# Optimization experiments

Measured on AMD Instinct MI355X. Metric: run time of the kernel, lower is better.

## Reference

```python
import jax, jax.numpy as jnp
import numpy as np
import math

B, N, CS, CZ = 1, 1024, 384, 128
H, G, PQ, PV = 8, 16, 8, 12
C = 3 * G              # c_hidden = group_dim * 3 = 48
CZ4 = CZ // 4
INF, EPS = 1e5, 1e-8


def _quat_to_rot(q):
    # q: [..., 4] -> [..., 3, 3] valid rotation matrices
    q = q / jnp.linalg.norm(q, axis=-1, keepdims=True)
    w, x, y, z = q[..., 0], q[..., 1], q[..., 2], q[..., 3]
    r = jnp.stack([
        1 - 2 * (y * y + z * z), 2 * (x * y - w * z), 2 * (x * z + w * y),
        2 * (x * y + w * z), 1 - 2 * (x * x + z * z), 2 * (y * z - w * x),
        2 * (x * z - w * y), 2 * (y * z + w * x), 1 - 2 * (x * x + y * y)], axis=-1)
    return r.reshape(q.shape[:-1] + (3, 3))


def setup_inputs() -> dict:
    key = jax.random.key(0)
    ks = jax.random.split(key, 12)
    sc = lambda d: 1.0 / math.sqrt(d)
    inp = {
        's': jax.random.normal(ks[0], (B, N, CS), jnp.float32),
        'z': jax.random.normal(ks[1], (B, N, N, CZ), jnp.float32),
        'rot': _quat_to_rot(jax.random.normal(ks[2], (B, N, 4), jnp.float32)),
        'mask': jnp.ones((B, N), jnp.float32),
        'wq': jax.random.normal(ks[3], (CS, H * C), jnp.float32) * sc(CS),
        'bq': jnp.zeros((H * C,), jnp.float32),
        'wkv': jax.random.normal(ks[4], (CS, 2 * H * C), jnp.float32) * sc(CS),
        'bkv': jnp.zeros((2 * H * C,), jnp.float32),
        'wkvp': jax.random.normal(ks[5], (CS, H * (PQ + PV) * 3), jnp.float32) * sc(CS),
        'bkvp': jnp.zeros((H * (PQ + PV) * 3,), jnp.float32),
        'wb': jax.random.normal(ks[6], (CZ, H), jnp.float32) * sc(CZ),
        'bb': jnp.zeros((H,), jnp.float32),
        'wdz': jax.random.normal(ks[7], (CZ, CZ4), jnp.float32) * sc(CZ),
        'bdz': jnp.zeros((CZ4,), jnp.float32),
        'wout': jax.random.normal(ks[8], (H * (CZ4 + C + 4 * PV), CS), jnp.float32) * sc(H * (CZ4 + C + 4 * PV)),
        'bout': jnp.zeros((CS,), jnp.float32),
        # ipa_point_weights_init_ -> softplus_inverse(1.0) = log(e-1); add jitter
        'gw': jnp.full((G,), float(np.log(np.e - 1.0)), jnp.float32) + 0.1 * jax.random.normal(ks[9], (G,), jnp.float32),
    }
    return inp


def reference(s, z, rot, mask, wq, bq, wkv, bkv, wkvp, bkvp, wb, bb, wdz, bdz, wout, bout, gw):
    # scalar q/k/v: [B,N,H,C]
    q = (s @ wq + bq).reshape(B, N, H, C)
    kv = (s @ wkv + bkv).reshape(B, N, H, 2 * C)
    k, v = kv[..., :C], kv[..., C:]

    # kv points: split last dim into 3 coordinate chunks, stack on -1 (per source)
    kvp = (s @ wkvp + bkvp).reshape(B, N, 3, H * (PQ + PV))
    kvp = jnp.moveaxis(kvp, -2, -1).reshape(B, N, H, PQ + PV, 3)
    v_pts = kvp[..., PQ:, :]  # [B,N,H,PV,3]; note: NOT rigid-transformed in source

    # pair bias [B,N,N,H]
    b = z @ wb + bb

    # groupwise 3D-RoPE: rotate per-residue 3D groups by frame rotation
    q_rot = jnp.einsum('bnij,bnhgj->bnhgi', rot, q.reshape(B, N, H, G, 3))
    k_rot = jnp.einsum('bnij,bnhgj->bnhgi', rot, k.reshape(B, N, H, G, 3))
    gs = jnp.einsum('bnhgi,bmhgi->bhgnm', q_rot, k_rot) / math.sqrt(3.0)  # [B,H,G,N,N]
    hw = jax.nn.softplus(gw) * math.sqrt(1.0 / G)  # [G]
    a = jnp.einsum('bhgnm,g->bhnm', gs, hw)
    a = a + math.sqrt(1.0 / 3.0) * jnp.transpose(b, (0, 3, 1, 2))

    sq_mask = INF * (mask[:, :, None] * mask[:, None, :] - 1.0)  # [B,N,N]
    a = jax.nn.softmax(a + sq_mask[:, None], axis=-1)  # [B,H,N,N]

    # scalar output
    o = jnp.einsum('bhnm,bmhc->bnhc', a, v).reshape(B, N, H * C)
    # point output
    o_pt = jnp.einsum('bhnm,bmhpc->bnhpc', a, v_pts)  # [B,N,H,PV,3]
    o_pt_norm = jnp.sqrt(jnp.sum(o_pt ** 2, axis=-1) + EPS).reshape(B, N, H * PV)
    o_pt = o_pt.reshape(B, N, H * PV, 3)
    # pair output
    pair_z = z @ wdz + bdz  # [B,N,N,CZ4]
    o_pair = jnp.einsum('bhnm,bnmd->bnhd', a, pair_z).reshape(B, N, H * CZ4)

    feats = jnp.concatenate([o, o_pt[..., 0], o_pt[..., 1], o_pt[..., 2], o_pt_norm, o_pair], axis=-1)
    return feats @ wout + bout
```

## Files before the change

### kernel.cpp

```cpp
#include <hip/hip_runtime.h>
#include <math.h>

#define NRES 1024
#define HH 8
#define CC 48
#define CZF 128

__global__ __launch_bounds__(256) void k_proj(
    const float* __restrict__ s,
    const float* __restrict__ wq, const float* __restrict__ bq,
    const float* __restrict__ wkv, const float* __restrict__ bkv,
    const float* __restrict__ wkvp, const float* __restrict__ bkvp,
    float* __restrict__ raw)
{
  int bb = blockIdx.x;
  int n0 = (bb >> 1) * 8;
  int ch = bb & 1;
  int t = threadIdx.x;
  const float* srow = s + (size_t)n0 * 384;
  for (int ci = 0; ci < 4; ci++) {
    int local = ci * 256 + t;
    if (local >= 816) break;
    int col = ch * 816 + local;
    const float* w; int ld; float bias;
    if (col < 384)       { w = wq  + col;          ld = 384; bias = bq[col]; }
    else if (col < 1152) { w = wkv + (col - 384);  ld = 768; bias = bkv[col - 384]; }
    else                 { w = wkvp + (col - 1152); ld = 480; bias = bkvp[col - 1152]; }
    float acc[8];
#pragma unroll
    for (int r = 0; r < 8; r++) acc[r] = bias;
    for (int k = 0; k < 384; k++) {
      float wv = w[(size_t)k * ld];
#pragma unroll
      for (int r = 0; r < 8; r++) acc[r] = fmaf(srow[r * 384 + k], wv, acc[r]);
    }
#pragma unroll
    for (int r = 0; r < 8; r++) raw[(size_t)(n0 + r) * 1632 + col] = acc[r];
  }
}

__global__ __launch_bounds__(256) void k_scatter(
    const float* __restrict__ raw, const float* __restrict__ rot,
    const float* __restrict__ gw,
    float* __restrict__ qp, float* __restrict__ kp, float* __restrict__ V2)
{
  int n = blockIdx.x, t = threadIdx.x;
  __shared__ float rsh[1632];
  __shared__ float hwsh[16];
  for (int i = t; i < 1632; i += 256) rsh[i] = raw[(size_t)n * 1632 + i];
  if (t < 16) hwsh[t] = log1pf(expf(gw[t])) * 0.25f;
  __syncthreads();
  float r00 = rot[n*9+0], r01 = rot[n*9+1], r02 = rot[n*9+2];
  float r10 = rot[n*9+3], r11 = rot[n*9+4], r12 = rot[n*9+5];
  float r20 = rot[n*9+6], r21 = rot[n*9+7], r22 = rot[n*9+8];
  for (int idx = t; idx < 768; idx += 256) {
    int isK = idx >= 384;
    int rem = idx - (isK ? 384 : 0);
    int h = rem / 48, gi = rem % 48, g = gi / 3, ii = gi % 3;
    int cb = isK ? (384 + h * 96 + g * 3) : (h * 48 + g * 3);
    float x = rsh[cb], y = rsh[cb + 1], zz = rsh[cb + 2];
    float d0 = r00 * x + r01 * y + r02 * zz;
    float d1 = r10 * x + r11 * y + r12 * zz;
    float d2 = r20 * x + r21 * y + r22 * zz;
    float val = (ii == 0) ? d0 : (ii == 1 ? d1 : d2);
    if (!isK) {
      val *= hwsh[g] * 0.57735026919f;
      qp[(size_t)((h << 10) + n) * 48 + gi] = val;
    } else {
      kp[(size_t)((h << 10) + n) * 48 + gi] = val;
    }
  }
  for (int idx = t; idx < 768; idx += 256) {
    int h = idx / 96, c = idx % 96;
    float val = 0.f;
    if (c < 48) val = rsh[384 + h * 96 + 48 + c];
    else if (c < 84) {
      int pc = c - 48, pp = pc / 3, j = pc % 3;
      val = rsh[1152 + j * 160 + h * 20 + 8 + pp];
    }
    V2[(size_t)((h << 10) + n) * 96 + c] = val;
  }
}

__global__ __launch_bounds__(256) void k_bias(
    const float* __restrict__ z, const float* __restrict__ wb,
    const float* __restrict__ bb, const float* __restrict__ mask,
    float* __restrict__ S)
{
  __shared__ float zsh[8192];
  __shared__ float wbrep[4128];
  __shared__ float bbsh[8];
  int t = threadIdx.x;
  size_t pair0 = (size_t)blockIdx.x * 64;
  for (int idx = t; idx < 1024; idx += 256) {
    float v = wb[idx];
    wbrep[idx] = v; wbrep[1032 + idx] = v; wbrep[2064 + idx] = v; wbrep[3096 + idx] = v;
  }
  if (t < 8) bbsh[t] = bb[t];
  const float4* z4 = (const float4*)(z + pair0 * 128);
#pragma unroll
  for (int it = 0; it < 8; it++) {
    int idx = it * 256 + t;
    float4 f = z4[idx];
    int r = idx >> 5, c = (idx & 31) * 4;
    *(float4*)&zsh[r * 128 + ((c + 4 * r) & 127)] = f;
  }
  __syncthreads();
  int q = t & 3, r = t >> 2;
  float acc[8];
#pragma unroll
  for (int hh = 0; hh < 8; hh++) acc[hh] = 0.f;
  const float* wbq = wbrep + q * 1032;
#pragma unroll
  for (int i = 0; i < 8; i++) {
    int c = q * 4 + i * 16;
    float4 zf = *(const float4*)&zsh[r * 128 + ((c + 4 * r) & 127)];
#pragma unroll
    for (int j = 0; j < 4; j++) {
      float zv = (j == 0) ? zf.x : (j == 1) ? zf.y : (j == 2) ? zf.z : zf.w;
      float4 w0 = *(const float4*)&wbq[(c + j) * 8];
      float4 w1 = *(const float4*)&wbq[(c + j) * 8 + 4];
      acc[0] = fmaf(zv, w0.x, acc[0]); acc[1] = fmaf(zv, w0.y, acc[1]);
      acc[2] = fmaf(zv, w0.z, acc[2]); acc[3] = fmaf(zv, w0.w, acc[3]);
      acc[4] = fmaf(zv, w1.x, acc[4]); acc[5] = fmaf(zv, w1.y, acc[5]);
      acc[6] = fmaf(zv, w1.z, acc[6]); acc[7] = fmaf(zv, w1.w, acc[7]);
    }
  }
#pragma unroll
  for (int hh = 0; hh < 8; hh++) {
    acc[hh] += __shfl_xor(acc[hh], 1, 64);
    acc[hh] += __shfl_xor(acc[hh], 2, 64);
  }
  size_t pair = pair0 + r;
  int n = (int)(pair >> 10), m = (int)(pair & 1023);
  float mt = 100000.0f * (mask[n] * mask[m] - 1.0f);
  const float is3 = 0.57735026919f;
  int h0 = q * 2;
  S[(size_t)h0 * 1048576 + pair]       = (acc[h0] + bbsh[h0]) * is3 + mt;
  S[(size_t)(h0 + 1) * 1048576 + pair] = (acc[h0 + 1] + bbsh[h0 + 1]) * is3 + mt;
}

__global__ __launch_bounds__(256) void k_attn(
    const float* __restrict__ qp, const float* __restrict__ kp,
    float* __restrict__ S)
{
  int b = blockIdx.x;
  int h = b >> 7, n0 = (b & 127) * 8;
  int t = threadIdx.x;
  __shared__ float ksh[128 * 52];
  __shared__ float ssh[8 * 1024];
  int ms = t & 127, nh = t >> 7;
  const float* qbase = qp + (size_t)((h << 10) + n0 + nh * 4) * 48;
  size_t Sbase = (size_t)h * 1048576 + (size_t)n0 * 1024;
  for (int cb = 0; cb < 1024; cb += 128) {
    __syncthreads();
    for (int idx = t; idx < 1536; idx += 256) {
      int r = idx / 12, p = idx % 12;
      float4 f = *(const float4*)(kp + (size_t)((h << 10) + cb + r) * 48 + p * 4);
      *(float4*)&ksh[r * 52 + p * 4] = f;
    }
    __syncthreads();
    int m = cb + ms;
    float a0 = 0.f, a1 = 0.f, a2 = 0.f, a3 = 0.f;
#pragma unroll
    for (int ic = 0; ic < 12; ic++) {
      float4 kf = *(const float4*)&ksh[ms * 52 + ic * 4];
      float4 q0 = *(const float4*)(qbase + 0 * 48 + ic * 4);
      float4 q1 = *(const float4*)(qbase + 1 * 48 + ic * 4);
      float4 q2 = *(const float4*)(qbase + 2 * 48 + ic * 4);
      float4 q3 = *(const float4*)(qbase + 3 * 48 + ic * 4);
      a0 += q0.x * kf.x + q0.y * kf.y + q0.z * kf.z + q0.w * kf.w;
      a1 += q1.x * kf.x + q1.y * kf.y + q1.z * kf.z + q1.w * kf.w;
      a2 += q2.x * kf.x + q2.y * kf.y + q2.z * kf.z + q2.w * kf.w;
      a3 += q3.x * kf.x + q3.y * kf.y + q3.z * kf.z + q3.w * kf.w;
    }
    int rb = nh * 4;
    ssh[(rb + 0) * 1024 + m] = a0 + S[Sbase + (size_t)(rb + 0) * 1024 + m];
    ssh[(rb + 1) * 1024 + m] = a1 + S[Sbase + (size_t)(rb + 1) * 1024 + m];
    ssh[(rb + 2) * 1024 + m] = a2 + S[Sbase + (size_t)(rb + 2) * 1024 + m];
    ssh[(rb + 3) * 1024 + m] = a3 + S[Sbase + (size_t)(rb + 3) * 1024 + m];
  }
  __syncthreads();
  int row = t >> 5, lane = t & 31;
  float* sr = ssh + row * 1024;
  float mx = -1e30f;
  for (int j = lane; j < 1024; j += 32) mx = fmaxf(mx, sr[j]);
#pragma unroll
  for (int o = 16; o >= 1; o >>= 1) mx = fmaxf(mx, __shfl_xor(mx, o, 32));
  float sum = 0.f;
  for (int j = lane; j < 1024; j += 32) {
    float e = __expf(sr[j] - mx);
    sr[j] = e; sum += e;
  }
#pragma unroll
  for (int o = 16; o >= 1; o >>= 1) sum += __shfl_xor(sum, o, 32);
  float inv = 1.0f / sum;
  float* Sout = S + Sbase + (size_t)row * 1024;
  for (int j = lane; j < 1024; j += 32) Sout[j] = sr[j] * inv;
}

__global__ __launch_bounds__(256) void k_av(
    const float* __restrict__ S, const float* __restrict__ V2,
    float* __restrict__ F)
{
  int b = blockIdx.x;
  int h = b >> 6, n0 = (b & 63) * 16;
  int t = threadIdx.x;
  __shared__ float as2[64 * 20];
  __shared__ float fsh[16 * 96];
  int np = t >> 5, c4 = t & 31;
  float4 a0 = {0,0,0,0}, a1 = {0,0,0,0};
  size_t Sbase = (size_t)h * 1048576 + (size_t)n0 * 1024;
  for (int mc = 0; mc < 1024; mc += 64) {
    __syncthreads();
    for (int idx = t; idx < 1024; idx += 256) {
      int mm = idx & 63, nn = idx >> 6;
      as2[mm * 20 + nn] = S[Sbase + (size_t)nn * 1024 + mc + mm];
    }
    __syncthreads();
    if (c4 < 24) {
      const float* vbase = V2 + (size_t)((h << 10) + mc) * 96 + c4 * 4;
      for (int mm = 0; mm < 64; mm++) {
        float4 vv = *(const float4*)(vbase + mm * 96);
        float2 av = *(const float2*)&as2[mm * 20 + np * 2];
        a0.x += av.x * vv.x; a0.y += av.x * vv.y; a0.z += av.x * vv.z; a0.w += av.x * vv.w;
        a1.x += av.y * vv.x; a1.y += av.y * vv.y; a1.z += av.y * vv.z; a1.w += av.y * vv.w;
      }
    }
  }
  if (c4 < 24) {
    *(float4*)&fsh[(np * 2 + 0) * 96 + c4 * 4] = a0;
    *(float4*)&fsh[(np * 2 + 1) * 96 + c4 * 4] = a1;
  }
  __syncthreads();
  for (int idx = t; idx < 768; idx += 256) {
    int nn = idx / 48, c = idx % 48;
    F[(size_t)(n0 + nn) * 1024 + h * 48 + c] = fsh[nn * 96 + c];
  }
  for (int idx = t; idx < 192; idx += 256) {
    int nn = idx / 12, pp = idx % 12;
    float x = fsh[nn * 96 + 48 + pp * 3];
    float y = fsh[nn * 96 + 48 + pp * 3 + 1];
    float zz = fsh[nn * 96 + 48 + pp * 3 + 2];
    size_t base = (size_t)(n0 + nn) * 1024;
    F[base + 384 + h * 12 + pp] = x;
    F[base + 480 + h * 12 + pp] = y;
    F[base + 576 + h * 12 + pp] = zz;
    F[base + 672 + h * 12 + pp] = sqrtf(x * x + y * y + zz * zz + 1e-8f);
  }
}

__global__ __launch_bounds__(256) void k_az(
    const float* __restrict__ S, const float* __restrict__ z,
    float* __restrict__ tmp)
{
  int n = blockIdx.x, t = threadIdx.x;
  __shared__ float zsh[8192];
  __shared__ float as2[64 * 12];
  int mg = t >> 5, c4 = t & 31;
  float4 acc[8];
#pragma unroll
  for (int hh = 0; hh < 8; hh++) acc[hh] = {0,0,0,0};
  for (int mc = 0; mc < 1024; mc += 64) {
    __syncthreads();
    const float4* z4 = (const float4*)(z + ((size_t)n * 1024 + mc) * 128);
#pragma unroll
    for (int it = 0; it < 8; it++) {
      int idx = it * 256 + t;
      float4 f = z4[idx];
      int r = idx >> 5, c = (idx & 31) * 4;
      *(float4*)&zsh[r * 128 + ((c + 4 * r) & 127)] = f;
    }
    for (int idx = t; idx < 512; idx += 256) {
      int mm = idx & 63, hh = idx >> 6;
      as2[mm * 12 + hh] = S[(size_t)hh * 1048576 + (size_t)n * 1024 + mc + mm];
    }
    __syncthreads();
#pragma unroll
    for (int k2 = 0; k2 < 8; k2++) {
      int mm = mg + k2 * 8;
      float4 zf = *(const float4*)&zsh[mm * 128 + ((c4 * 4 + 4 * mm) & 127)];
      float4 av0 = *(const float4*)&as2[mm * 12];
      float4 av1 = *(const float4*)&as2[mm * 12 + 4];
      acc[0].x += av0.x*zf.x; acc[0].y += av0.x*zf.y; acc[0].z += av0.x*zf.z; acc[0].w += av0.x*zf.w;
      acc[1].x += av0.y*zf.x; acc[1].y += av0.y*zf.y; acc[1].z += av0.y*zf.z; acc[1].w += av0.y*zf.w;
      acc[2].x += av0.z*zf.x; acc[2].y += av0.z*zf.y; acc[2].z += av0.z*zf.z; acc[2].w += av0.z*zf.w;
      acc[3].x += av0.w*zf.x; acc[3].y += av0.w*zf.y; acc[3].z += av0.w*zf.z; acc[3].w += av0.w*zf.w;
      acc[4].x += av1.x*zf.x; acc[4].y += av1.x*zf.y; acc[4].z += av1.x*zf.z; acc[4].w += av1.x*zf.w;
      acc[5].x += av1.y*zf.x; acc[5].y += av1.y*zf.y; acc[5].z += av1.y*zf.z; acc[5].w += av1.y*zf.w;
      acc[6].x += av1.z*zf.x; acc[6].y += av1.z*zf.y; acc[6].z += av1.z*zf.z; acc[6].w += av1.z*zf.w;
      acc[7].x += av1.w*zf.x; acc[7].y += av1.w*zf.y; acc[7].z += av1.w*zf.z; acc[7].w += av1.w*zf.w;
    }
  }
  __syncthreads();
#pragma unroll
  for (int hh = 0; hh < 8; hh++)
    *(float4*)&zsh[mg * 1024 + hh * 128 + c4 * 4] = acc[hh];
  __syncthreads();
  for (int idx = t; idx < 1024; idx += 256) {
    float sv = 0.f;
#pragma unroll
    for (int g2 = 0; g2 < 8; g2++) sv += zsh[g2 * 1024 + idx];
    tmp[(size_t)n * 1024 + idx] = sv;
  }
}

__global__ __launch_bounds__(256) void k_out(
    const float* __restrict__ F, const float* __restrict__ tmp,
    const float* __restrict__ wdz, const float* __restrict__ bdz,
    const float* __restrict__ wout, const float* __restrict__ bout,
    float* __restrict__ out)
{
  int n0 = blockIdx.x * 4, t = threadIdx.x;
  __shared__ float fsh[4 * 1024];
  for (int idx = t; idx < 3072; idx += 256) {
    int nn = idx / 768, c = idx % 768;
    fsh[nn * 1024 + c] = F[(size_t)(n0 + nn) * 1024 + c];
  }
  {
    int h = t >> 5, d = t & 31;
#pragma unroll
    for (int nn = 0; nn < 4; nn++) {
      float acc = bdz[d];
      const float* tr = tmp + (size_t)(n0 + nn) * 1024 + h * 128;
      for (int c = 0; c < 128; c++) acc = fmaf(tr[c], wdz[c * 32 + d], acc);
      fsh[nn * 1024 + 768 + h * 32 + d] = acc;
    }
  }
  __syncthreads();
  int j = t & 127, kh = t >> 7;
  float a[3][4];
#pragma unroll
  for (int jj = 0; jj < 3; jj++)
#pragma unroll
    for (int r = 0; r < 4; r++) a[jj][r] = 0.f;
  const float4* f4p = (const float4*)fsh;
  for (int k4 = kh * 128; k4 < kh * 128 + 128; k4++) {
    float4 f0 = f4p[0 * 256 + k4];
    float4 f1 = f4p[1 * 256 + k4];
    float4 f2 = f4p[2 * 256 + k4];
    float4 f3 = f4p[3 * 256 + k4];
    int k = k4 * 4;
#pragma unroll
    for (int u = 0; u < 4; u++) {
      float w0 = wout[(size_t)(k + u) * 384 + j];
      float w1 = wout[(size_t)(k + u) * 384 + j + 128];
      float w2 = wout[(size_t)(k + u) * 384 + j + 256];
      float e0 = (u == 0) ? f0.x : (u == 1) ? f0.y : (u == 2) ? f0.z : f0.w;
      float e1 = (u == 0) ? f1.x : (u == 1) ? f1.y : (u == 2) ? f1.z : f1.w;
      float e2 = (u == 0) ? f2.x : (u == 1) ? f2.y : (u == 2) ? f2.z : f2.w;
      float e3 = (u == 0) ? f3.x : (u == 1) ? f3.y : (u == 2) ? f3.z : f3.w;
      a[0][0] = fmaf(e0, w0, a[0][0]); a[0][1] = fmaf(e1, w0, a[0][1]);
      a[0][2] = fmaf(e2, w0, a[0][2]); a[0][3] = fmaf(e3, w0, a[0][3]);
      a[1][0] = fmaf(e0, w1, a[1][0]); a[1][1] = fmaf(e1, w1, a[1][1]);
      a[1][2] = fmaf(e2, w1, a[1][2]); a[1][3] = fmaf(e3, w1, a[1][3]);
      a[2][0] = fmaf(e0, w2, a[2][0]); a[2][1] = fmaf(e1, w2, a[2][1]);
      a[2][2] = fmaf(e2, w2, a[2][2]); a[2][3] = fmaf(e3, w2, a[2][3]);
    }
  }
  __syncthreads();
  if (kh == 1) {
#pragma unroll
    for (int jj = 0; jj < 3; jj++)
#pragma unroll
      for (int r = 0; r < 4; r++)
        fsh[(jj * 4 + r) * 128 + j] = a[jj][r];
  }
  __syncthreads();
  if (kh == 0) {
#pragma unroll
    for (int jj = 0; jj < 3; jj++)
#pragma unroll
      for (int r = 0; r < 4; r++) {
        float v = a[jj][r] + fsh[(jj * 4 + r) * 128 + j] + bout[jj * 128 + j];
        out[(size_t)(n0 + r) * 384 + jj * 128 + j] = v;
      }
  }
}

extern "C" void kernel_launch(void* const* d_in, const int* in_sizes, int n_in,
                              void* d_out, int out_size, void* d_ws, size_t ws_size,
                              hipStream_t stream) {
  const float* s    = (const float*)d_in[0];
  const float* z    = (const float*)d_in[1];
  const float* rot  = (const float*)d_in[2];
  const float* mask = (const float*)d_in[3];
  const float* wq   = (const float*)d_in[4];
  const float* bq   = (const float*)d_in[5];
  const float* wkv  = (const float*)d_in[6];
  const float* bkv  = (const float*)d_in[7];
  const float* wkvp = (const float*)d_in[8];
  const float* bkvp = (const float*)d_in[9];
  const float* wb   = (const float*)d_in[10];
  const float* bb   = (const float*)d_in[11];
  const float* wdz  = (const float*)d_in[12];
  const float* bdz  = (const float*)d_in[13];
  const float* wout = (const float*)d_in[14];
  const float* bout = (const float*)d_in[15];
  const float* gw   = (const float*)d_in[16];
  float* out = (float*)d_out;

  float* ws  = (float*)d_ws;
  float* raw = ws;
  float* qp  = raw + 1024 * 1632;
  float* kp  = qp + 393216;
  float* V2  = kp + 393216;
  float* S   = V2 + 786432;
  float* tmp = S + 8388608;
  float* F   = tmp + 1048576;

  k_proj<<<256, 256, 0, stream>>>(s, wq, bq, wkv, bkv, wkvp, bkvp, raw);
  k_scatter<<<1024, 256, 0, stream>>>(raw, rot, gw, qp, kp, V2);
  k_bias<<<16384, 256, 0, stream>>>(z, wb, bb, mask, S);
  k_attn<<<1024, 256, 0, stream>>>(qp, kp, S);
  k_av<<<512, 256, 0, stream>>>(S, V2, F);
  k_az<<<1024, 256, 0, stream>>>(S, z, tmp);
  k_out<<<256, 256, 0, stream>>>(F, tmp, wdz, bdz, wout, bout, out);
}
```

Baseline: 1.326 ms.

## Rework grids and staging across proj, bias, av, az and out kernels

Splits k_proj and k_out over twice as many blocks to raise parallelism. k_bias now reads z straight from global memory instead of staging it through shared memory, with each thread handling four pairs, and shrinks the replicated weight table. k_av stages the whole attention row block transposed in LDS once, and k_az stages all head attention weights once and streams z directly from global, which removes the per-chunk barriers. The bigger LDS footprint in k_av (about 74KB) lowers occupancy, and the direct global z loads give up the coalesced shared-memory staging.

```diff
diff --git a/kernel.cpp b/kernel.cpp
--- a/kernel.cpp
+++ b/kernel.cpp
@@ -14,14 +14,14 @@
     float* __restrict__ raw)
 {
   int bb = blockIdx.x;
-  int n0 = (bb >> 1) * 8;
-  int ch = bb & 1;
+  int n0 = (bb >> 2) * 8;
+  int ch = bb & 3;
   int t = threadIdx.x;
   const float* srow = s + (size_t)n0 * 384;
-  for (int ci = 0; ci < 4; ci++) {
+  for (int ci = 0; ci < 2; ci++) {
     int local = ci * 256 + t;
-    if (local >= 816) break;
-    int col = ch * 816 + local;
+    if (local >= 408) break;
+    int col = ch * 408 + local;
     const float* w; int ld; float bias;
     if (col < 384)       { w = wq  + col;          ld = 384; bias = bq[col]; }
     else if (col < 1152) { w = wkv + (col - 384);  ld = 768; bias = bkv[col - 384]; }
@@ -87,57 +87,74 @@
     const float* __restrict__ bb, const float* __restrict__ mask,
     float* __restrict__ S)
 {
-  __shared__ float zsh[8192];
-  __shared__ float wbrep[4128];
+  __shared__ float wbrep[2][1032];
   __shared__ float bbsh[8];
   int t = threadIdx.x;
-  size_t pair0 = (size_t)blockIdx.x * 64;
+  size_t pair0 = (size_t)blockIdx.x * 256;
   for (int idx = t; idx < 1024; idx += 256) {
     float v = wb[idx];
-    wbrep[idx] = v; wbrep[1032 + idx] = v; wbrep[2064 + idx] = v; wbrep[3096 + idx] = v;
+    wbrep[0][idx] = v; wbrep[1][idx] = v;
   }
   if (t < 8) bbsh[t] = bb[t];
-  const float4* z4 = (const float4*)(z + pair0 * 128);
-#pragma unroll
-  for (int it = 0; it < 8; it++) {
-    int idx = it * 256 + t;
-    float4 f = z4[idx];
-    int r = idx >> 5, c = (idx & 31) * 4;
-    *(float4*)&zsh[r * 128 + ((c + 4 * r) & 127)] = f;
-  }
   __syncthreads();
   int q = t & 3, r = t >> 2;
-  float acc[8];
-#pragma unroll
-  for (int hh = 0; hh < 8; hh++) acc[hh] = 0.f;
-  const float* wbq = wbrep + q * 1032;
+  const float* wbq = wbrep[q >> 1];
+  float acc[4][8];
+#pragma unroll
+  for (int g = 0; g < 4; g++)
+#pragma unroll
+    for (int hh = 0; hh < 8; hh++) acc[g][hh] = 0.f;
+  const float* zb = z + (pair0 + r) * 128;
 #pragma unroll
   for (int i = 0; i < 8; i++) {
     int c = q * 4 + i * 16;
-    float4 zf = *(const float4*)&zsh[r * 128 + ((c + 4 * r) & 127)];
+    float4 zf0 = *(const float4*)(zb + (size_t)0 * 8192 + c);
+    float4 zf1 = *(const float4*)(zb + (size_t)1 * 8192 + c);
+    float4 zf2 = *(const float4*)(zb + (size_t)2 * 8192 + c);
+    float4 zf3 = *(const float4*)(zb + (size_t)3 * 8192 + c);
 #pragma unroll
     for (int j = 0; j < 4; j++) {
-      float zv = (j == 0) ? zf.x : (j == 1) ? zf.y : (j == 2) ? zf.z : zf.w;
       float4 w0 = *(const float4*)&wbq[(c + j) * 8];
       float4 w1 = *(const float4*)&wbq[(c + j) * 8 + 4];
-      acc[0] = fmaf(zv, w0.x, acc[0]); acc[1] = fmaf(zv, w0.y, acc[1]);
-      acc[2] = fmaf(zv, w0.z, acc[2]); acc[3] = fmaf(zv, w0.w, acc[3]);
-      acc[4] = fmaf(zv, w1.x, acc[4]); acc[5] = fmaf(zv, w1.y, acc[5]);
-      acc[6] = fmaf(zv, w1.z, acc[6]); acc[7] = fmaf(zv, w1.w, acc[7]);
-    }
-  }
-#pragma unroll
-  for (int hh = 0; hh < 8; hh++) {
-    acc[hh] += __shfl_xor(acc[hh], 1, 64);
-    acc[hh] += __shfl_xor(acc[hh], 2, 64);
-  }
-  size_t pair = pair0 + r;
-  int n = (int)(pair >> 10), m = (int)(pair & 1023);
-  float mt = 100000.0f * (mask[n] * mask[m] - 1.0f);
+      float z0 = (j == 0) ? zf0.x : (j == 1) ? zf0.y : (j == 2) ? zf0.z : zf0.w;
+      float z1 = (j == 0) ? zf1.x : (j == 1) ? zf1.y : (j == 2) ? zf1.z : zf1.w;
+      float z2 = (j == 0) ? zf2.x : (j == 1) ? zf2.y : (j == 2) ? zf2.z : zf2.w;
+      float z3 = (j == 0) ? zf3.x : (j == 1) ? zf3.y : (j == 2) ? zf3.z : zf3.w;
+      acc[0][0] = fmaf(z0, w0.x, acc[0][0]); acc[0][1] = fmaf(z0, w0.y, acc[0][1]);
+      acc[0][2] = fmaf(z0, w0.z, acc[0][2]); acc[0][3] = fmaf(z0, w0.w, acc[0][3]);
+      acc[0][4] = fmaf(z0, w1.x, acc[0][4]); acc[0][5] = fmaf(z0, w1.y, acc[0][5]);
+      acc[0][6] = fmaf(z0, w1.z, acc[0][6]); acc[0][7] = fmaf(z0, w1.w, acc[0][7]);
+      acc[1][0] = fmaf(z1, w0.x, acc[1][0]); acc[1][1] = fmaf(z1, w0.y, acc[1][1]);
+      acc[1][2] = fmaf(z1, w0.z, acc[1][2]); acc[1][3] = fmaf(z1, w0.w, acc[1][3]);
+      acc[1][4] = fmaf(z1, w1.x, acc[1][4]); acc[1][5] = fmaf(z1, w1.y, acc[1][5]);
+      acc[1][6] = fmaf(z1, w1.z, acc[1][6]); acc[1][7] = fmaf(z1, w1.w, acc[1][7]);
+      acc[2][0] = fmaf(z2, w0.x, acc[2][0]); acc[2][1] = fmaf(z2, w0.y, acc[2][1]);
+      acc[2][2] = fmaf(z2, w0.z, acc[2][2]); acc[2][3] = fmaf(z2, w0.w, acc[2][3]);
+      acc[2][4] = fmaf(z2, w1.x, acc[2][4]); acc[2][5] = fmaf(z2, w1.y, acc[2][5]);
+      acc[2][6] = fmaf(z2, w1.z, acc[2][6]); acc[2][7] = fmaf(z2, w1.w, acc[2][7]);
+      acc[3][0] = fmaf(z3, w0.x, acc[3][0]); acc[3][1] = fmaf(z3, w0.y, acc[3][1]);
+      acc[3][2] = fmaf(z3, w0.z, acc[3][2]); acc[3][3] = fmaf(z3, w0.w, acc[3][3]);
+      acc[3][4] = fmaf(z3, w1.x, acc[3][4]); acc[3][5] = fmaf(z3, w1.y, acc[3][5]);
+      acc[3][6] = fmaf(z3, w1.z, acc[3][6]); acc[3][7] = fmaf(z3, w1.w, acc[3][7]);
+    }
+  }
+#pragma unroll
+  for (int g = 0; g < 4; g++)
+#pragma unroll
+    for (int hh = 0; hh < 8; hh++) {
+      acc[g][hh] += __shfl_xor(acc[g][hh], 1, 64);
+      acc[g][hh] += __shfl_xor(acc[g][hh], 2, 64);
+    }
   const float is3 = 0.57735026919f;
   int h0 = q * 2;
-  S[(size_t)h0 * 1048576 + pair]       = (acc[h0] + bbsh[h0]) * is3 + mt;
-  S[(size_t)(h0 + 1) * 1048576 + pair] = (acc[h0 + 1] + bbsh[h0 + 1]) * is3 + mt;
+#pragma unroll
+  for (int g = 0; g < 4; g++) {
+    size_t pair = pair0 + r + (size_t)g * 64;
+    int n = (int)(pair >> 10), m = (int)(pair & 1023);
+    float mt = 100000.0f * (mask[n] * mask[m] - 1.0f);
+    S[(size_t)h0 * 1048576 + pair]       = (acc[g][h0] + bbsh[h0]) * is3 + mt;
+    S[(size_t)(h0 + 1) * 1048576 + pair] = (acc[g][h0 + 1] + bbsh[h0 + 1]) * is3 + mt;
+  }
 }
 
 __global__ __launch_bounds__(256) void k_attn(
@@ -206,29 +223,25 @@
   int b = blockIdx.x;
   int h = b >> 6, n0 = (b & 63) * 16;
   int t = threadIdx.x;
-  __shared__ float as2[64 * 20];
+  __shared__ float asT[1024 * 18];
   __shared__ float fsh[16 * 96];
+  size_t Sbase = (size_t)h * 1048576 + (size_t)n0 * 1024;
+  for (int idx = t; idx < 16384; idx += 256) {
+    int nn = idx >> 10, m = idx & 1023;
+    asT[m * 18 + nn] = S[Sbase + (size_t)nn * 1024 + m];
+  }
+  __syncthreads();
   int np = t >> 5, c4 = t & 31;
   float4 a0 = {0,0,0,0}, a1 = {0,0,0,0};
-  size_t Sbase = (size_t)h * 1048576 + (size_t)n0 * 1024;
-  for (int mc = 0; mc < 1024; mc += 64) {
-    __syncthreads();
-    for (int idx = t; idx < 1024; idx += 256) {
-      int mm = idx & 63, nn = idx >> 6;
-      as2[mm * 20 + nn] = S[Sbase + (size_t)nn * 1024 + mc + mm];
-    }
-    __syncthreads();
-    if (c4 < 24) {
-      const float* vbase = V2 + (size_t)((h << 10) + mc) * 96 + c4 * 4;
-      for (int mm = 0; mm < 64; mm++) {
-        float4 vv = *(const float4*)(vbase + mm * 96);
-        float2 av = *(const float2*)&as2[mm * 20 + np * 2];
-        a0.x += av.x * vv.x; a0.y += av.x * vv.y; a0.z += av.x * vv.z; a0.w += av.x * vv.w;
-        a1.x += av.y * vv.x; a1.y += av.y * vv.y; a1.z += av.y * vv.z; a1.w += av.y * vv.w;
-      }
-    }
-  }
   if (c4 < 24) {
+    const float* vbase = V2 + (size_t)(h << 10) * 96 + c4 * 4;
+#pragma unroll 4
+    for (int mm = 0; mm < 1024; mm++) {
+      float4 vv = *(const float4*)(vbase + (size_t)mm * 96);
+      float2 av = *(const float2*)&asT[mm * 18 + np * 2];
+      a0.x += av.x * vv.x; a0.y += av.x * vv.y; a0.z += av.x * vv.z; a0.w += av.x * vv.w;
+      a1.x += av.y * vv.x; a1.y += av.y * vv.y; a1.z += av.y * vv.z; a1.w += av.y * vv.w;
+    }
     *(float4*)&fsh[(np * 2 + 0) * 96 + c4 * 4] = a0;
     *(float4*)&fsh[(np * 2 + 1) * 96 + c4 * 4] = a1;
   }
@@ -255,52 +268,41 @@
     float* __restrict__ tmp)
 {
   int n = blockIdx.x, t = threadIdx.x;
-  __shared__ float zsh[8192];
-  __shared__ float as2[64 * 12];
+  __shared__ float ash[8192];
   int mg = t >> 5, c4 = t & 31;
+  for (int idx = t; idx < 8192; idx += 256) {
+    int hh = idx >> 10, m = idx & 1023;
+    ash[m * 8 + hh] = S[(size_t)hh * 1048576 + (size_t)n * 1024 + m];
+  }
+  __syncthreads();
   float4 acc[8];
 #pragma unroll
-  for (int hh = 0; hh < 8; hh++) acc[hh] = {0,0,0,0};
-  for (int mc = 0; mc < 1024; mc += 64) {
-    __syncthreads();
-    const float4* z4 = (const float4*)(z + ((size_t)n * 1024 + mc) * 128);
-#pragma unroll
-    for (int it = 0; it < 8; it++) {
-      int idx = it * 256 + t;
-      float4 f = z4[idx];
-      int r = idx >> 5, c = (idx & 31) * 4;
-      *(float4*)&zsh[r * 128 + ((c + 4 * r) & 127)] = f;
-    }
-    for (int idx = t; idx < 512; idx += 256) {
-      int mm = idx & 63, hh = idx >> 6;
-      as2[mm * 12 + hh] = S[(size_t)hh * 1048576 + (size_t)n * 1024 + mc + mm];
-    }
-    __syncthreads();
-#pragma unroll
-    for (int k2 = 0; k2 < 8; k2++) {
-      int mm = mg + k2 * 8;
-      float4 zf = *(const float4*)&zsh[mm * 128 + ((c4 * 4 + 4 * mm) & 127)];
-      float4 av0 = *(const float4*)&as2[mm * 12];
-      float4 av1 = *(const float4*)&as2[mm * 12 + 4];
-      acc[0].x += av0.x*zf.x; acc[0].y += av0.x*zf.y; acc[0].z += av0.x*zf.z; acc[0].w += av0.x*zf.w;
-      acc[1].x += av0.y*zf.x; acc[1].y += av0.y*zf.y; acc[1].z += av0.y*zf.z; acc[1].w += av0.y*zf.w;
-      acc[2].x += av0.z*zf.x; acc[2].y += av0.z*zf.y; acc[2].z += av0.z*zf.z; acc[2].w += av0.z*zf.w;
-      acc[3].x += av0.w*zf.x; acc[3].y += av0.w*zf.y; acc[3].z += av0.w*zf.z; acc[3].w += av0.w*zf.w;
-      acc[4].x += av1.x*zf.x; acc[4].y += av1.x*zf.y; acc[4].z += av1.x*zf.z; acc[4].w += av1.x*zf.w;
-      acc[5].x += av1.y*zf.x; acc[5].y += av1.y*zf.y; acc[5].z += av1.y*zf.z; acc[5].w += av1.y*zf.w;
-      acc[6].x += av1.z*zf.x; acc[6].y += av1.z*zf.y; acc[6].z += av1.z*zf.z; acc[6].w += av1.z*zf.w;
-      acc[7].x += av1.w*zf.x; acc[7].y += av1.w*zf.y; acc[7].z += av1.w*zf.z; acc[7].w += av1.w*zf.w;
-    }
+  for (int hh = 0; hh < 8; hh++) acc[hh] = {0.f, 0.f, 0.f, 0.f};
+  const float4* zn = (const float4*)(z + (size_t)n * 131072);
+#pragma unroll 4
+  for (int k2 = 0; k2 < 128; k2++) {
+    int mm = k2 * 8 + mg;
+    float4 zf = zn[mm * 32 + c4];
+    float4 av0 = *(const float4*)&ash[mm * 8];
+    float4 av1 = *(const float4*)&ash[mm * 8 + 4];
+    acc[0].x += av0.x*zf.x; acc[0].y += av0.x*zf.y; acc[0].z += av0.x*zf.z; acc[0].w += av0.x*zf.w;
+    acc[1].x += av0.y*zf.x; acc[1].y += av0.y*zf.y; acc[1].z += av0.y*zf.z; acc[1].w += av0.y*zf.w;
+    acc[2].x += av0.z*zf.x; acc[2].y += av0.z*zf.y; acc[2].z += av0.z*zf.z; acc[2].w += av0.z*zf.w;
+    acc[3].x += av0.w*zf.x; acc[3].y += av0.w*zf.y; acc[3].z += av0.w*zf.z; acc[3].w += av0.w*zf.w;
+    acc[4].x += av1.x*zf.x; acc[4].y += av1.x*zf.y; acc[4].z += av1.x*zf.z; acc[4].w += av1.x*zf.w;
+    acc[5].x += av1.y*zf.x; acc[5].y += av1.y*zf.y; acc[5].z += av1.y*zf.z; acc[5].w += av1.y*zf.w;
+    acc[6].x += av1.z*zf.x; acc[6].y += av1.z*zf.y; acc[6].z += av1.z*zf.z; acc[6].w += av1.z*zf.w;
+    acc[7].x += av1.w*zf.x; acc[7].y += av1.w*zf.y; acc[7].z += av1.w*zf.z; acc[7].w += av1.w*zf.w;
   }
   __syncthreads();
 #pragma unroll
   for (int hh = 0; hh < 8; hh++)
-    *(float4*)&zsh[mg * 1024 + hh * 128 + c4 * 4] = acc[hh];
+    *(float4*)&ash[mg * 1024 + hh * 128 + c4 * 4] = acc[hh];
   __syncthreads();
   for (int idx = t; idx < 1024; idx += 256) {
     float sv = 0.f;
 #pragma unroll
-    for (int g2 = 0; g2 < 8; g2++) sv += zsh[g2 * 1024 + idx];
+    for (int g2 = 0; g2 < 8; g2++) sv += ash[g2 * 1024 + idx];
     tmp[(size_t)n * 1024 + idx] = sv;
   }
 }
@@ -311,16 +313,16 @@
     const float* __restrict__ wout, const float* __restrict__ bout,
     float* __restrict__ out)
 {
-  int n0 = blockIdx.x * 4, t = threadIdx.x;
-  __shared__ float fsh[4 * 1024];
-  for (int idx = t; idx < 3072; idx += 256) {
+  int n0 = blockIdx.x * 2, t = threadIdx.x;
+  __shared__ float fsh[2 * 1024];
+  for (int idx = t; idx < 1536; idx += 256) {
     int nn = idx / 768, c = idx % 768;
     fsh[nn * 1024 + c] = F[(size_t)(n0 + nn) * 1024 + c];
   }
   {
     int h = t >> 5, d = t & 31;
 #pragma unroll
-    for (int nn = 0; nn < 4; nn++) {
+    for (int nn = 0; nn < 2; nn++) {
       float acc = bdz[d];
       const float* tr = tmp + (size_t)(n0 + nn) * 1024 + h * 128;
       for (int c = 0; c < 128; c++) acc = fmaf(tr[c], wdz[c * 32 + d], acc);
@@ -329,17 +331,15 @@
   }
   __syncthreads();
   int j = t & 127, kh = t >> 7;
-  float a[3][4];
+  float a[3][2];
 #pragma unroll
   for (int jj = 0; jj < 3; jj++)
 #pragma unroll
-    for (int r = 0; r < 4; r++) a[jj][r] = 0.f;
+    for (int r = 0; r < 2; r++) a[jj][r] = 0.f;
   const float4* f4p = (const float4*)fsh;
   for (int k4 = kh * 128; k4 < kh * 128 + 128; k4++) {
-    float4 f0 = f4p[0 * 256 + k4];
-    float4 f1 = f4p[1 * 256 + k4];
-    float4 f2 = f4p[2 * 256 + k4];
-    float4 f3 = f4p[3 * 256 + k4];
+    float4 f0 = f4p[k4];
+    float4 f1 = f4p[256 + k4];
     int k = k4 * 4;
 #pragma unroll
     for (int u = 0; u < 4; u++) {
@@ -348,14 +348,9 @@
       float w2 = wout[(size_t)(k + u) * 384 + j + 256];
       float e0 = (u == 0) ? f0.x : (u == 1) ? f0.y : (u == 2) ? f0.z : f0.w;
       float e1 = (u == 0) ? f1.x : (u == 1) ? f1.y : (u == 2) ? f1.z : f1.w;
-      float e2 = (u == 0) ? f2.x : (u == 1) ? f2.y : (u == 2) ? f2.z : f2.w;
-      float e3 = (u == 0) ? f3.x : (u == 1) ? f3.y : (u == 2) ? f3.z : f3.w;
       a[0][0] = fmaf(e0, w0, a[0][0]); a[0][1] = fmaf(e1, w0, a[0][1]);
-      a[0][2] = fmaf(e2, w0, a[0][2]); a[0][3] = fmaf(e3, w0, a[0][3]);
       a[1][0] = fmaf(e0, w1, a[1][0]); a[1][1] = fmaf(e1, w1, a[1][1]);
-      a[1][2] = fmaf(e2, w1, a[1][2]); a[1][3] = fmaf(e3, w1, a[1][3]);
       a[2][0] = fmaf(e0, w2, a[2][0]); a[2][1] = fmaf(e1, w2, a[2][1]);
-      a[2][2] = fmaf(e2, w2, a[2][2]); a[2][3] = fmaf(e3, w2, a[2][3]);
     }
   }
   __syncthreads();
@@ -363,16 +358,16 @@
 #pragma unroll
     for (int jj = 0; jj < 3; jj++)
 #pragma unroll
-      for (int r = 0; r < 4; r++)
-        fsh[(jj * 4 + r) * 128 + j] = a[jj][r];
+      for (int r = 0; r < 2; r++)
+        fsh[(jj * 2 + r) * 128 + j] = a[jj][r];
   }
   __syncthreads();
   if (kh == 0) {
 #pragma unroll
     for (int jj = 0; jj < 3; jj++)
 #pragma unroll
-      for (int r = 0; r < 4; r++) {
-        float v = a[jj][r] + fsh[(jj * 4 + r) * 128 + j] + bout[jj * 128 + j];
+      for (int r = 0; r < 2; r++) {
+        float v = a[jj][r] + fsh[(jj * 2 + r) * 128 + j] + bout[jj * 128 + j];
         out[(size_t)(n0 + r) * 384 + jj * 128 + j] = v;
       }
   }
@@ -409,11 +404,11 @@
   float* tmp = S + 8388608;
   float* F   = tmp + 1048576;
 
-  k_proj<<<256, 256, 0, stream>>>(s, wq, bq, wkv, bkv, wkvp, bkvp, raw);
+  k_proj<<<512, 256, 0, stream>>>(s, wq, bq, wkv, bkv, wkvp, bkvp, raw);
   k_scatter<<<1024, 256, 0, stream>>>(raw, rot, gw, qp, kp, V2);
-  k_bias<<<16384, 256, 0, stream>>>(z, wb, bb, mask, S);
+  k_bias<<<4096, 256, 0, stream>>>(z, wb, bb, mask, S);
   k_attn<<<1024, 256, 0, stream>>>(qp, kp, S);
   k_av<<<512, 256, 0, stream>>>(S, V2, F);
   k_az<<<1024, 256, 0, stream>>>(S, z, tmp);
-  k_out<<<256, 256, 0, stream>>>(F, tmp, wdz, bdz, wout, bout, out);
-}
+  k_out<<<512, 256, 0, stream>>>(F, tmp, wdz, bdz, wout, bout, out);
+}
```

After: 1.212 ms. -8.6%, faster.
